# Performance work log

Measured on AMD Instinct MI355X. Metric: run time of the kernel, lower is better.

The kernel has to match this reference:

```python
import jax, jax.numpy as jnp
import numpy as np

N = 4096
C = 128
L = 4
E = 131072
HEADS = 4
BN_EPS = 1e-5


def setup_inputs() -> dict:
    key = jax.random.key(0)
    ks = jax.random.split(key, 16)
    s = jnp.float32(0.05)

    def rn(k, shape):
        return jax.random.normal(k, shape, dtype=jnp.float32) * s

    return {
        "x": jax.random.normal(ks[0], (N, C), dtype=jnp.float32),
        "edge_index": jax.random.randint(ks[1], (2, E), 0, N, dtype=jnp.int64) if jax.config.read("jax_enable_x64") else jax.random.randint(ks[1], (2, E), 0, N, dtype=jnp.int32),
        "gin_w1": rn(ks[2], (L, C, C)), "gin_b1": jnp.zeros((L, C), jnp.float32),
        "gin_w2": rn(ks[3], (L, C, C)), "gin_b2": jnp.zeros((L, C), jnp.float32),
        "attn_in_w": rn(ks[4], (L, 3 * C, C)), "attn_in_b": jnp.zeros((L, 3 * C), jnp.float32),
        "attn_out_w": rn(ks[5], (L, C, C)), "attn_out_b": jnp.zeros((L, C), jnp.float32),
        "n1_g": jnp.ones((L, C), jnp.float32), "n1_b": jnp.zeros((L, C), jnp.float32),
        "n2_g": jnp.ones((L, C), jnp.float32), "n2_b": jnp.zeros((L, C), jnp.float32),
        "n3_g": jnp.ones((L, C), jnp.float32), "n3_b": jnp.zeros((L, C), jnp.float32),
        "mlp_w1": rn(ks[6], (L, 2 * C, C)), "mlp_b1": jnp.zeros((L, 2 * C), jnp.float32),
        "mlp_w2": rn(ks[7], (L, C, 2 * C)), "mlp_b2": jnp.zeros((L, C), jnp.float32),
        "head_w1": rn(ks[8], (C // 2, C)), "head_b1": jnp.zeros((C // 2,), jnp.float32),
        "head_w2": rn(ks[9], (C // 4, C // 2)), "head_b2": jnp.zeros((C // 4,), jnp.float32),
        "head_w3": rn(ks[10], (1, C // 4)), "head_b3": jnp.zeros((1,), jnp.float32),
    }


def _bn(x, g, b):
    # BatchNorm1d over the node dim, training-mode (biased var), eps=1e-5
    mu = x.mean(axis=0)
    var = x.var(axis=0)
    return g * (x - mu) * jax.lax.rsqrt(var + BN_EPS) + b


def _gin(x, src, dst, w1, b1, w2, b2):
    # GINConv with eps=0: nn(x + sum_{j in N(i)} x_j)
    agg = jax.ops.segment_sum(x[src], dst, num_segments=x.shape[0])
    h = x + agg
    h = jnp.maximum(h @ w1.T + b1, 0.0)
    return h @ w2.T + b2


def _mha(x, wi, bi, wo, bo):
    # torch.nn.MultiheadAttention self-attention over a single dense batch of N nodes
    n, c = x.shape
    d = c // HEADS
    q, k, v = jnp.split(x @ wi.T + bi, 3, axis=-1)
    q = q.reshape(n, HEADS, d)
    k = k.reshape(n, HEADS, d)
    v = v.reshape(n, HEADS, d)
    scores = jnp.einsum('nhd,mhd->hnm', q, k) / jnp.sqrt(jnp.asarray(d, x.dtype))
    a = jax.nn.softmax(scores, axis=-1)
    o = jnp.einsum('hnm,mhd->nhd', a, v).reshape(n, c)
    return o @ wo.T + bo


def _forward(x, edge_index, gin_w1, gin_b1, gin_w2, gin_b2, attn_in_w, attn_in_b,
             attn_out_w, attn_out_b, n1_g, n1_b, n2_g, n2_b, n3_g, n3_b,
             mlp_w1, mlp_b1, mlp_w2, mlp_b2, head_w1, head_b1, head_w2, head_b2,
             head_w3, head_b3):
    src, dst = edge_index[0], edge_index[1]
    for i in range(L):
        # local GIN branch + residual + batch norm
        h1 = _bn(_gin(x, src, dst, gin_w1[i], gin_b1[i], gin_w2[i], gin_b2[i]) + x, n1_g[i], n1_b[i])
        # global attention branch + residual + batch norm
        h2 = _bn(_mha(x, attn_in_w[i], attn_in_b[i], attn_out_w[i], attn_out_b[i]) + x, n2_g[i], n2_b[i])
        h = h1 + h2
        # GPSConv MLP (C -> 2C -> C) with residual and final batch norm
        m = jnp.maximum(h @ mlp_w1[i].T + mlp_b1[i], 0.0) @ mlp_w2[i].T + mlp_b2[i]
        x = _bn(h + m, n3_g[i], n3_b[i])
    # head MLP: C -> C/2 -> C/4 -> 1
    h = jnp.maximum(x @ head_w1.T + head_b1, 0.0)
    h = jnp.maximum(h @ head_w2.T + head_b2, 0.0)
    return h @ head_w3.T + head_b3


def reference(x, edge_index, gin_w1, gin_b1, gin_w2, gin_b2, attn_in_w, attn_in_b,
              attn_out_w, attn_out_b, n1_g, n1_b, n2_g, n2_b, n3_g, n3_b,
              mlp_w1, mlp_b1, mlp_w2, mlp_b2, head_w1, head_b1, head_w2, head_b2,
              head_w3, head_b3):
    return _forward(x, edge_index, gin_w1, gin_b1, gin_w2, gin_b2, attn_in_w, attn_in_b,
                    attn_out_w, attn_out_b, n1_g, n1_b, n2_g, n2_b, n3_g, n3_b,
                    mlp_w1, mlp_b1, mlp_w2, mlp_b2, head_w1, head_b1, head_w2, head_b2,
                    head_w3, head_b3)
```

## Files before the change

kernel.cpp:

```cpp
#include <hip/hip_runtime.h>

#define N_NODES 4096
#define C_DIM   128
#define L_LAYERS 4
#define E_EDGES 131072
#define H_HEADS 4
#define D_HEAD  32
#define NC      (N_NODES * C_DIM)
#define NCu     (N_NODES * C_DIM)
#define P_STRIDE 136
#define HS_STRIDE 152
#define T2S       264

typedef short bf16x8 __attribute__((ext_vector_type(8)));
typedef float f32x4  __attribute__((ext_vector_type(4)));

__device__ __forceinline__ unsigned short f2bf(float f) {
    unsigned int u = __float_as_uint(f);
    u += 0x7fffu + ((u >> 16) & 1u);
    return (unsigned short)(u >> 16);
}

__device__ __forceinline__ float bf_lo(unsigned int u) { return __uint_as_float(u << 16); }
__device__ __forceinline__ float bf_hi(unsigned int u) { return __uint_as_float(u & 0xffff0000u); }

__device__ __forceinline__ bf16x8 pack8(const float* v) {
    bf16x8 o;
#pragma unroll
    for (int i = 0; i < 8; ++i) o[i] = (short)f2bf(v[i]);
    return o;
}

__global__ __launch_bounds__(256) void hist_kernel(const int* __restrict__ ei,
                                                   int* __restrict__ deg) {
    int e = blockIdx.x * 256 + threadIdx.x;
    atomicAdd(&deg[ei[E_EDGES + e]], 1);
}

__global__ __launch_bounds__(256) void scan_kernel(const int* __restrict__ deg,
                                                   int* __restrict__ rowstart,
                                                   int* __restrict__ cursor) {
    __shared__ int ts[256];
    const int tid = threadIdx.x;
    int loc[16];
    int s = 0;
#pragma unroll
    for (int i = 0; i < 16; ++i) { loc[i] = s; s += deg[tid * 16 + i]; }
    ts[tid] = s;
    __syncthreads();
    for (int off = 1; off < 256; off <<= 1) {
        int t = (tid >= off) ? ts[tid - off] : 0;
        __syncthreads();
        if (tid >= off) ts[tid] += t;
        __syncthreads();
    }
    int off0 = ts[tid] - s;
#pragma unroll
    for (int i = 0; i < 16; ++i) {
        int v = off0 + loc[i];
        rowstart[tid * 16 + i] = v;
        cursor[tid * 16 + i] = v;
    }
    if (tid == 255) rowstart[4096] = off0 + s;
}

__global__ __launch_bounds__(256) void fill_kernel(const int* __restrict__ ei,
                                                   int* __restrict__ cursor,
                                                   int* __restrict__ csr_src) {
    int e = blockIdx.x * 256 + threadIdx.x;
    int d = ei[E_EDGES + e];
    int s = ei[e];
    int p = atomicAdd(&cursor[d], 1);
    csr_src[p] = s;
}

__global__ __launch_bounds__(256) void wcvt(const float* __restrict__ s0, const float* __restrict__ s1,
                                            const float* __restrict__ s2, const float* __restrict__ s3,
                                            const float* __restrict__ s4, const float* __restrict__ s5,
                                            unsigned short* __restrict__ wbf) {
    int i0 = (blockIdx.x * 256 + threadIdx.x) * 8;
    const float* src; int base;
    if      (i0 < 65536)  { src = s0; base = 0; }
    else if (i0 < 131072) { src = s1; base = 65536; }
    else if (i0 < 327680) { src = s2; base = 131072; }
    else if (i0 < 393216) { src = s3; base = 327680; }
    else if (i0 < 524288) { src = s4; base = 393216; }
    else                  { src = s5; base = 524288; }
    const float* p = src + (i0 - base);
    float t[8];
#pragma unroll
    for (int i = 0; i < 8; ++i) t[i] = p[i];
    *(bf16x8*)(wbf + i0) = pack8(t);
}

__global__ __launch_bounds__(256) void x2bf(const float* __restrict__ x,
                                            unsigned short* __restrict__ xb) {
    int i0 = (blockIdx.x * 256 + threadIdx.x) * 8;
    float t[8];
#pragma unroll
    for (int i = 0; i < 8; ++i) t[i] = x[i0 + i];
    *(bf16x8*)(xb + i0) = pack8(t);
}

__global__ __launch_bounds__(256, 8) void qkv_gather(const unsigned short* __restrict__ xb,
                                                     const unsigned short* __restrict__ Wbf,
                                                     const float* __restrict__ bias,
                                                     unsigned short* __restrict__ Qb,
                                                     unsigned short* __restrict__ Kb,
                                                     unsigned short* __restrict__ VT,
                                                     const int* __restrict__ rowstart,
                                                     const int* __restrict__ csr_src,
                                                     unsigned int* __restrict__ hsum,
                                                     float* __restrict__ ssz) {
    const int b = blockIdx.x;
    const int tid = threadIdx.x;
    if (b < 1536) {
        const int ct = b % 6, rt = b / 6;
        const int wv = tid >> 6;
        const int lane = tid & 63, lg = lane >> 4, ll = lane & 15;
        const int rowbase = rt * 16;
        const int colbase = ct * 64 + wv * 16;

        const unsigned short* Ap = xb  + (size_t)(rowbase + ll) * 128 + lg * 8;
        const unsigned short* Wp = Wbf + (size_t)(colbase + ll) * 128 + lg * 8;

        f32x4 acc = {0.f, 0.f, 0.f, 0.f};
#pragma unroll
        for (int k = 0; k < 128; k += 32) {
            bf16x8 a = *(const bf16x8*)(Ap + k);
            bf16x8 w = *(const bf16x8*)(Wp + k);
            acc = __builtin_amdgcn_mfma_f32_16x16x32_bf16(a, w, acc, 0, 0, 0);
        }

        const float qsc = 0.25506973f;
        const int col = colbase + ll;
        const float bi = bias[col];
#pragma unroll
        for (int r = 0; r < 4; ++r) {
            const int row = rowbase + lg * 4 + r;
            float v = acc[r] + bi;
            if (col < 128) {
                int hh = col >> 5, d = col & 31;
                Qb[((size_t)hh * N_NODES + row) * D_HEAD + d] = f2bf(v * qsc);
            } else if (col < 256) {
                int c2 = col - 128, hh = c2 >> 5, d = c2 & 31;
                Kb[((size_t)hh * N_NODES + row) * D_HEAD + d] = f2bf(v);
            } else {
                int c2 = col - 256, hh = c2 >> 5, d = c2 & 31;
                VT[((size_t)hh * D_HEAD + d) * N_NODES + row] = f2bf(v);
            }
        }
    } else {
        if (b == 1536) {
            ssz[tid] = 0.f; ssz[256 + tid] = 0.f; ssz[512 + tid] = 0.f;
        }
        const int node = (b - 1536) * 4 + (tid >> 6);
        const int lane = tid & 63;
        const unsigned int* xu = (const unsigned int*)xb;
        const int beg = rowstart[node], end = rowstart[node + 1];
        unsigned int su = xu[(size_t)node * 64 + lane];
        float ax = bf_lo(su), ay = bf_hi(su);
        float bx = 0.f, by = 0.f;
        int e = beg;
        for (; e + 4 <= end; e += 4) {
            int s0 = csr_src[e], s1 = csr_src[e + 1], s2 = csr_src[e + 2], s3 = csr_src[e + 3];
            unsigned int u0 = xu[(size_t)s0 * 64 + lane];
            unsigned int u1 = xu[(size_t)s1 * 64 + lane];
            unsigned int u2 = xu[(size_t)s2 * 64 + lane];
            unsigned int u3 = xu[(size_t)s3 * 64 + lane];
            ax += bf_lo(u0) + bf_lo(u1); ay += bf_hi(u0) + bf_hi(u1);
            bx += bf_lo(u2) + bf_lo(u3); by += bf_hi(u2) + bf_hi(u3);
        }
        for (; e < end; ++e) {
            unsigned int u0 = xu[(size_t)csr_src[e] * 64 + lane];
            ax += bf_lo(u0); ay += bf_hi(u0);
        }
        float ox = ax + bx, oy = ay + by;
        hsum[(size_t)node * 64 + lane] = (unsigned int)f2bf(ox) | ((unsigned int)f2bf(oy) << 16);
    }
}

__global__ __launch_bounds__(512, 4) void attn_gin1(const unsigned short* __restrict__ Qb,
                                                    const unsigned short* __restrict__ Kb,
                                                    const unsigned short* __restrict__ VT,
                                                    unsigned short* __restrict__ ob,
                                                    const unsigned short* __restrict__ hsum,
                                                    const unsigned short* __restrict__ W1,
                                                    const float* __restrict__ bias1,
                                                    unsigned short* __restrict__ t1out) {
    __shared__ __align__(16) unsigned short Pl[8 * 32 * P_STRIDE];
    float (*Ouns)[32][33] = (float (*)[32][33])(void*)Pl;
    float (*Llp)[32] = (float (*)[32])(void*)(Pl + 8 * 32 * 33 * 2);

    const int b   = blockIdx.x;
    const int tid = threadIdx.x;
    const int wv  = tid >> 6;
    const int lane = tid & 63;
    const int lg  = lane >> 4;
    const int ll  = lane & 15;

    if (b >= 512) {
        const int rowbase = (b - 512) * 16;
        const int colbase = wv * 16;
        const unsigned short* Ap = hsum + (size_t)(rowbase + ll) * 128 + lg * 8;
        const unsigned short* Wp = W1 + (size_t)(colbase + ll) * 128 + lg * 8;
        f32x4 acc = {0.f, 0.f, 0.f, 0.f};
#pragma unroll
        for (int k = 0; k < 128; k += 32) {
            bf16x8 a = *(const bf16x8*)(Ap + k);
            bf16x8 w = *(const bf16x8*)(Wp + k);
            acc = __builtin_amdgcn_mfma_f32_16x16x32_bf16(a, w, acc, 0, 0, 0);
        }
        const int col = colbase + ll;
        const float bi = bias1[col];
#pragma unroll
        for (int r = 0; r < 4; ++r) {
            const int row = rowbase + lg * 4 + r;
            float v = fmaxf(acc[r] + bi, 0.f);
            t1out[(size_t)row * 128 + col] = f2bf(v);
        }
        return;
    }

    const int h   = b >> 7;
    const int q0  = (b & 127) * 32;

    const unsigned short* Qh = Qb + ((size_t)h * N_NODES + q0) * D_HEAD;
    const unsigned short* Kh = Kb + (size_t)h * N_NODES * D_HEAD;
    const unsigned short* Vh = VT + (size_t)h * D_HEAD * N_NODES;

    bf16x8 qf0 = *(const bf16x8*)(Qh + ll * D_HEAD + lg * 8);
    bf16x8 qf1 = *(const bf16x8*)(Qh + (16 + ll) * D_HEAD + lg * 8);

    f32x4 oacc00 = {0.f,0.f,0.f,0.f}, oacc01 = {0.f,0.f,0.f,0.f};
    f32x4 oacc10 = {0.f,0.f,0.f,0.f}, oacc11 = {0.f,0.f,0.f,0.f};
    float l0[4] = {0.f,0.f,0.f,0.f}, l1[4] = {0.f,0.f,0.f,0.f};

    unsigned short* Pw = Pl + wv * (32 * P_STRIDE);
    const int k0 = wv * (N_NODES / 8);

    for (int t = 0; t < (N_NODES / 8) / 128; ++t) {
        const int kt = k0 + t * 128;

        float s0[8][4], s1[8][4];
#pragma unroll
        for (int kc = 0; kc < 8; ++kc) {
            bf16x8 kf = *(const bf16x8*)(Kh + (size_t)(kt + kc * 16 + ll) * D_HEAD + lg * 8);
            f32x4 z = {0.f, 0.f, 0.f, 0.f};
            f32x4 d0 = __builtin_amdgcn_mfma_f32_16x16x32_bf16(qf0, kf, z, 0, 0, 0);
            f32x4 d1 = __builtin_amdgcn_mfma_f32_16x16x32_bf16(qf1, kf, z, 0, 0, 0);
#pragma unroll
            for (int r = 0; r < 4; ++r) { s0[kc][r] = d0[r]; s1[kc][r] = d1[r]; }
        }

#pragma unroll
        for (int r = 0; r < 4; ++r) {
            float a = 0.f, bb = 0.f;
#pragma unroll
            for (int kc = 0; kc < 8; ++kc) {
                float p0 = exp2f(s0[kc][r]); s0[kc][r] = p0; a += p0;
                float p1 = exp2f(s1[kc][r]); s1[kc][r] = p1; bb += p1;
            }
#pragma unroll
            for (int off = 1; off < 16; off <<= 1) {
                a += __shfl_xor(a, off, 64);
                bb += __shfl_xor(bb, off, 64);
            }
            l0[r] += a;
            l1[r] += bb;
        }

#pragma unroll
        for (int kc = 0; kc < 8; ++kc)
#pragma unroll
            for (int r = 0; r < 4; ++r) {
                Pw[(lg * 4 + r) * P_STRIDE + kc * 16 + ll]      = f2bf(s0[kc][r]);
                Pw[(16 + lg * 4 + r) * P_STRIDE + kc * 16 + ll] = f2bf(s1[kc][r]);
            }
        asm volatile("" ::: "memory");

#pragma unroll
        for (int kc2 = 0; kc2 < 4; ++kc2) {
            bf16x8 va = *(const bf16x8*)(Vh + (size_t)ll * N_NODES + kt + kc2 * 32 + lg * 8);
            bf16x8 vb = *(const bf16x8*)(Vh + (size_t)(16 + ll) * N_NODES + kt + kc2 * 32 + lg * 8);
            bf16x8 pf0 = *(const bf16x8*)(Pw + ll * P_STRIDE + kc2 * 32 + lg * 8);
            bf16x8 pf1 = *(const bf16x8*)(Pw + (16 + ll) * P_STRIDE + kc2 * 32 + lg * 8);
            oacc00 = __builtin_amdgcn_mfma_f32_16x16x32_bf16(pf0, va, oacc00, 0, 0, 0);
            oacc01 = __builtin_amdgcn_mfma_f32_16x16x32_bf16(pf0, vb, oacc01, 0, 0, 0);
            oacc10 = __builtin_amdgcn_mfma_f32_16x16x32_bf16(pf1, va, oacc10, 0, 0, 0);
            oacc11 = __builtin_amdgcn_mfma_f32_16x16x32_bf16(pf1, vb, oacc11, 0, 0, 0);
        }
    }

    __syncthreads();

#pragma unroll
    for (int r = 0; r < 4; ++r) {
        Ouns[wv][lg * 4 + r][ll]           = oacc00[r];
        Ouns[wv][lg * 4 + r][16 + ll]      = oacc01[r];
        Ouns[wv][16 + lg * 4 + r][ll]      = oacc10[r];
        Ouns[wv][16 + lg * 4 + r][16 + ll] = oacc11[r];
    }
    if (ll == 0) {
#pragma unroll
        for (int r = 0; r < 4; ++r) {
            Llp[wv][lg * 4 + r]      = l0[r];
            Llp[wv][16 + lg * 4 + r] = l1[r];
        }
    }
    __syncthreads();

    {
        const int row = tid >> 4, col = tid & 15;
        float L = 0.f, oa = 0.f, obv = 0.f;
#pragma unroll
        for (int w = 0; w < 8; ++w) {
            L   += Llp[w][row];
            oa  += Ouns[w][row][col];
            obv += Ouns[w][row][16 + col];
        }
        float inv = 1.f / L;
        ob[(size_t)(q0 + row) * C_DIM + h * D_HEAD + col]      = f2bf(oa * inv);
        ob[(size_t)(q0 + row) * C_DIM + h * D_HEAD + 16 + col] = f2bf(obv * inv);
    }
}

__global__ __launch_bounds__(256, 8) void gemm2x(const unsigned short* __restrict__ A0,
                                                 const unsigned short* __restrict__ W0,
                                                 const float* __restrict__ bias0,
                                                 float* __restrict__ out0,
                                                 float* __restrict__ stats0,
                                                 const unsigned short* __restrict__ A1,
                                                 const unsigned short* __restrict__ W1,
                                                 const float* __restrict__ bias1,
                                                 float* __restrict__ out1,
                                                 float* __restrict__ stats1,
                                                 const float* __restrict__ resid) {
    const int b = blockIdx.x;
    const int which = b >> 9;
    const int bl = b & 511;
    const unsigned short* Abf = which ? A1 : A0;
    const unsigned short* Wbf = which ? W1 : W0;
    const float* bias = which ? bias1 : bias0;
    float* outf  = which ? out1 : out0;
    float* stats = which ? stats1 : stats0;

    const int tid = threadIdx.x;
    const int wv = tid >> 6;
    const int lane = tid & 63, lg = lane >> 4, ll = lane & 15;
    const int rowbase = (bl >> 1) * 16;
    const int colbase = (bl & 1) * 64 + wv * 16;

    const unsigned short* Ap = Abf + (size_t)(rowbase + ll) * 128 + lg * 8;
    const unsigned short* Wp = Wbf + (size_t)(colbase + ll) * 128 + lg * 8;

    f32x4 acc = {0.f, 0.f, 0.f, 0.f};
#pragma unroll
    for (int k = 0; k < 128; k += 32) {
        bf16x8 a = *(const bf16x8*)(Ap + k);
        bf16x8 w = *(const bf16x8*)(Wp + k);
        acc = __builtin_amdgcn_mfma_f32_16x16x32_bf16(a, w, acc, 0, 0, 0);
    }

    const int col = colbase + ll;
    const float bi = bias[col];
    float sv = 0.f, sv2 = 0.f;
#pragma unroll
    for (int r = 0; r < 4; ++r) {
        const int row = rowbase + lg * 4 + r;
        float v = acc[r] + bi + resid[(size_t)row * 128 + col];
        outf[(size_t)row * 128 + col] = v;
        sv += v; sv2 += v * v;
    }
    sv  += __shfl_xor(sv, 16, 64);  sv  += __shfl_xor(sv, 32, 64);
    sv2 += __shfl_xor(sv2, 16, 64); sv2 += __shfl_xor(sv2, 32, 64);
    if (lg == 0) {
        atomicAdd(&stats[col], sv);
        atomicAdd(&stats[128 + col], sv2);
    }
}

__global__ __launch_bounds__(256) void mlp_fused(const float* __restrict__ g1p,
                                                 const float* __restrict__ a2p,
                                                 const float* __restrict__ st1,
                                                 const float* __restrict__ st2,
                                                 const float* __restrict__ g1v,
                                                 const float* __restrict__ b1v,
                                                 const float* __restrict__ g2v,
                                                 const float* __restrict__ b2v,
                                                 const unsigned short* __restrict__ W1bf,
                                                 const float* __restrict__ bias1,
                                                 const unsigned short* __restrict__ W2bf,
                                                 const float* __restrict__ bias2,
                                                 float* __restrict__ m3out,
                                                 float* __restrict__ stats3) {
    __shared__ float hf[16][132];
    __shared__ __align__(16) unsigned short hs[16 * HS_STRIDE];
    __shared__ __align__(16) unsigned short t2s[16 * T2S];
    __shared__ float scl[4][128];

    const int tid = threadIdx.x;
    const int rowbase = blockIdx.x * 16;
    const float inv_n = 1.f / N_NODES;

    if (tid < 128) {
        const int ch = tid;
        float m1 = st1[ch] * inv_n;
        float v1 = st1[128 + ch] * inv_n - m1 * m1;
        float r1 = rsqrtf(v1 + 1e-5f);
        float sc1 = g1v[ch] * r1;
        scl[0][ch] = sc1;
        scl[1][ch] = b1v[ch] - m1 * sc1;
        float m2 = st2[ch] * inv_n;
        float v2 = st2[128 + ch] * inv_n - m2 * m2;
        float r2 = rsqrtf(v2 + 1e-5f);
        float sc2 = g2v[ch] * r2;
        scl[2][ch] = sc2;
        scl[3][ch] = b2v[ch] - m2 * sc2;
    }
    __syncthreads();

#pragma unroll
    for (int j = tid; j < 512; j += 256) {
        const int r = j >> 5, cq = (j & 31) * 4;
        float4 v1 = *(const float4*)(g1p + (size_t)(rowbase + r) * 128 + cq);
        float4 v2 = *(const float4*)(a2p + (size_t)(rowbase + r) * 128 + cq);
        float h0 = v1.x * scl[0][cq]     + scl[1][cq]     + v2.x * scl[2][cq]     + scl[3][cq];
        float h1 = v1.y * scl[0][cq + 1] + scl[1][cq + 1] + v2.y * scl[2][cq + 1] + scl[3][cq + 1];
        float h2 = v1.z * scl[0][cq + 2] + scl[1][cq + 2] + v2.z * scl[2][cq + 2] + scl[3][cq + 2];
        float h3 = v1.w * scl[0][cq + 3] + scl[1][cq + 3] + v2.w * scl[2][cq + 3] + scl[3][cq + 3];
        hf[r][cq] = h0; hf[r][cq + 1] = h1; hf[r][cq + 2] = h2; hf[r][cq + 3] = h3;
        ushort4 u;
        u.x = f2bf(h0); u.y = f2bf(h1); u.z = f2bf(h2); u.w = f2bf(h3);
        *(ushort4*)(&hs[r * HS_STRIDE + cq]) = u;
    }
    __syncthreads();

    const int wv = tid >> 6;
    const int lane = tid & 63, lg = lane >> 4, ll = lane & 15;

#pragma unroll
    for (int ct = 0; ct < 4; ++ct) {
        const int colbase = wv * 16 + ct * 64;
        const unsigned short* Wp = W1bf + (size_t)(colbase + ll) * 128 + lg * 8;
        f32x4 acc = {0.f, 0.f, 0.f, 0.f};
#pragma unroll
        for (int k = 0; k < 128; k += 32) {
            bf16x8 a = *(const bf16x8*)(&hs[ll * HS_STRIDE + k + lg * 8]);
            bf16x8 w = *(const bf16x8*)(Wp + k);
            acc = __builtin_amdgcn_mfma_f32_16x16x32_bf16(a, w, acc, 0, 0, 0);
        }
        const int col = colbase + ll;
        const float bi = bias1[col];
#pragma unroll
        for (int r = 0; r < 4; ++r) {
            float v = fmaxf(acc[r] + bi, 0.f);
            t2s[(lg * 4 + r) * T2S + col] = f2bf(v);
        }
    }
    __syncthreads();

#pragma unroll
    for (int p = 0; p < 2; ++p) {
        const int colbase = p * 64 + wv * 16;
        const unsigned short* Wp = W2bf + (size_t)(colbase + ll) * 256 + lg * 8;
        f32x4 acc = {0.f, 0.f, 0.f, 0.f};
#pragma unroll
        for (int k = 0; k < 256; k += 32) {
            bf16x8 a = *(const bf16x8*)(&t2s[ll * T2S + k + lg * 8]);
            bf16x8 w = *(const bf16x8*)(Wp + k);
            acc = __builtin_amdgcn_mfma_f32_16x16x32_bf16(a, w, acc, 0, 0, 0);
        }
        const int col = colbase + ll;
        const float bi = bias2[col];
        float sv = 0.f, sv2 = 0.f;
#pragma unroll
        for (int r = 0; r < 4; ++r) {
            const int row = lg * 4 + r;
            float v = acc[r] + bi + hf[row][col];
            m3out[(size_t)(rowbase + row) * 128 + col] = v;
            sv += v; sv2 += v * v;
        }
        sv  += __shfl_xor(sv, 16, 64);  sv  += __shfl_xor(sv, 32, 64);
        sv2 += __shfl_xor(sv2, 16, 64); sv2 += __shfl_xor(sv2, 32, 64);
        if (lg == 0) {
            atomicAdd(&stats3[col], sv);
            atomicAdd(&stats3[128 + col], sv2);
        }
    }
}

__global__ __launch_bounds__(256) void bn_apply(const float* __restrict__ p,
                                                const float* __restrict__ st,
                                                const float* __restrict__ gv,
                                                const float* __restrict__ bv,
                                                float* __restrict__ out,
                                                unsigned short* __restrict__ outb) {
    int idx = blockIdx.x * 256 + threadIdx.x;
    int c4 = (idx & 31) * 4;
    const float inv_n = 1.f / N_NODES;
    float sc[4], sh[4];
#pragma unroll
    for (int c = 0; c < 4; ++c) {
        int ch = c4 + c;
        float m = st[ch] * inv_n;
        float vv = st[C_DIM + ch] * inv_n - m * m;
        float r = rsqrtf(vv + 1e-5f);
        sc[c] = gv[ch] * r; sh[c] = bv[ch] - m * sc[c];
    }
    float4 v = ((const float4*)p)[idx];
    float4 o;
    o.x = v.x * sc[0] + sh[0];
    o.y = v.y * sc[1] + sh[1];
    o.z = v.z * sc[2] + sh[2];
    o.w = v.w * sc[3] + sh[3];
    ((float4*)out)[idx] = o;
    ushort4 ub;
    ub.x = f2bf(o.x); ub.y = f2bf(o.y); ub.z = f2bf(o.z); ub.w = f2bf(o.w);
    *(ushort4*)(outb + (size_t)idx * 4) = ub;
}

__global__ __launch_bounds__(256) void head_fused(const float* __restrict__ x,
                                                  const float* __restrict__ w1,
                                                  const float* __restrict__ b1,
                                                  const float* __restrict__ w2,
                                                  const float* __restrict__ b2,
                                                  const float* __restrict__ w3,
                                                  const float* __restrict__ b3,
                                                  float* __restrict__ out) {
    __shared__ __align__(16) float xs[8][128];
    __shared__ __align__(16) float hs2[8][64];
    const int tid = threadIdx.x;
    const int n = tid >> 5;
    const int g = tid & 31;
    const int node0 = blockIdx.x * 8;

    {
        int r = tid >> 5, q = tid & 31;
        *(float4*)(&xs[r][q * 4]) = *(const float4*)(x + (size_t)(node0 + r) * 128 + q * 4);
    }
    __syncthreads();

    {
        float acc0 = b1[g], acc1 = b1[g + 32];
        const float* wa = w1 + (size_t)g * 128;
        const float* wb = w1 + (size_t)(g + 32) * 128;
#pragma unroll 8
        for (int k = 0; k < 128; k += 4) {
            float4 xv = *(const float4*)(&xs[n][k]);
            float4 va = *(const float4*)(wa + k);
            float4 vb = *(const float4*)(wb + k);
            acc0 += xv.x * va.x + xv.y * va.y + xv.z * va.z + xv.w * va.w;
            acc1 += xv.x * vb.x + xv.y * vb.y + xv.z * vb.z + xv.w * vb.w;
        }
        hs2[n][g]      = fmaxf(acc0, 0.f);
        hs2[n][g + 32] = fmaxf(acc1, 0.f);
    }
    __syncthreads();

    {
        float acc = b2[g];
        const float* wr = w2 + (size_t)g * 64;
#pragma unroll 8
        for (int k = 0; k < 64; k += 4) {
            float4 hv = *(const float4*)(&hs2[n][k]);
            float4 wv = *(const float4*)(wr + k);
            acc += hv.x * wv.x + hv.y * wv.y + hv.z * wv.z + hv.w * wv.w;
        }
        float t = fmaxf(acc, 0.f) * w3[g];
#pragma unroll
        for (int off = 1; off < 32; off <<= 1) t += __shfl_xor(t, off, 64);
        if (g == 0) out[node0 + n] = t + b3[0];
    }
}

extern "C" void kernel_launch(void* const* d_in, const int* in_sizes, int n_in,
                              void* d_out, int out_size, void* d_ws, size_t ws_size,
                              hipStream_t stream) {
    (void)in_sizes; (void)n_in; (void)out_size; (void)ws_size;
    const float* x_in   = (const float*)d_in[0];
    const int*   ei     = (const int*)d_in[1];
    const float* gin_w1 = (const float*)d_in[2];
    const float* gin_b1 = (const float*)d_in[3];
    const float* gin_w2 = (const float*)d_in[4];
    const float* gin_b2 = (const float*)d_in[5];
    const float* ain_w  = (const float*)d_in[6];
    const float* ain_b  = (const float*)d_in[7];
    const float* aout_w = (const float*)d_in[8];
    const float* aout_b = (const float*)d_in[9];
    const float* n1_g   = (const float*)d_in[10];
    const float* n1_b   = (const float*)d_in[11];
    const float* n2_g   = (const float*)d_in[12];
    const float* n2_b   = (const float*)d_in[13];
    const float* n3_g   = (const float*)d_in[14];
    const float* n3_b   = (const float*)d_in[15];
    const float* mlp_w1 = (const float*)d_in[16];
    const float* mlp_b1 = (const float*)d_in[17];
    const float* mlp_w2 = (const float*)d_in[18];
    const float* mlp_b2 = (const float*)d_in[19];
    const float* h_w1   = (const float*)d_in[20];
    const float* h_b1   = (const float*)d_in[21];
    const float* h_w2   = (const float*)d_in[22];
    const float* h_b2   = (const float*)d_in[23];
    const float* h_w3   = (const float*)d_in[24];
    const float* h_b3   = (const float*)d_in[25];

    float* f = (float*)d_ws;
    float* g1   = f;
    float* m3   = f;
    float* a2   = f + 1 * (size_t)NC;
    float* hbuf = f + 2 * (size_t)NC;
    float* xA   = f + 3 * (size_t)NC;
    float* xB   = f + 4 * (size_t)NC;
    unsigned short* R1  = (unsigned short*)(f + 5 * (size_t)NC);
    unsigned short* Qb      = R1;
    unsigned short* Kb      = R1 + (size_t)NCu;
    unsigned short* VT      = R1 + 2 * (size_t)NCu;
    unsigned short* R2      = R1 + 3 * (size_t)NCu;
    unsigned short* ao_bf   = R2;
    unsigned short* hsum_bf = (unsigned short*)a2;
    unsigned short* t1_bf   = (unsigned short*)hbuf;
    unsigned short* xbf     = R2 + (size_t)NCu;
    unsigned short* wbf     = xbf + (size_t)NCu;
    float* ss    = (float*)(wbf + 655360);
    int* ibase    = (int*)(ss + 768);
    int* deg      = ibase;
    int* rowstart = ibase + 4096;
    int* cursor   = ibase + 4096 + 4098;
    int* csr_src  = ibase + 4096 + 4098 + 4096;

    const int OG1 = 0, OG2 = 65536, OAI = 131072, OAO = 327680, OM1 = 393216, OM2 = 524288;

    hipMemsetAsync(deg, 0, 4096 * sizeof(int), stream);
    hist_kernel<<<E_EDGES / 256, 256, 0, stream>>>(ei, deg);
    scan_kernel<<<1, 256, 0, stream>>>(deg, rowstart, cursor);
    fill_kernel<<<E_EDGES / 256, 256, 0, stream>>>(ei, cursor, csr_src);
    wcvt<<<320, 256, 0, stream>>>(gin_w1, gin_w2, ain_w, aout_w, mlp_w1, mlp_w2, wbf);
    x2bf<<<NC / 2048, 256, 0, stream>>>(x_in, xbf);

    for (int i = 0; i < L_LAYERS; ++i) {
        const float* xin = (i == 0) ? x_in : ((i & 1) ? xA : xB);
        float* xout = (i & 1) ? xB : xA;
        const float* gb1 = gin_b1 + (size_t)i * C_DIM;
        const float* gb2 = gin_b2 + (size_t)i * C_DIM;
        const float* aib = ain_b + (size_t)i * 3 * C_DIM;
        const float* aob = aout_b + (size_t)i * C_DIM;
        const float* mb1 = mlp_b1 + (size_t)i * 2 * C_DIM;
        const float* mb2 = mlp_b2 + (size_t)i * C_DIM;

        qkv_gather<<<2560, 256, 0, stream>>>(xbf, wbf + OAI + (size_t)i * 49152, aib,
                                             Qb, Kb, VT, rowstart, csr_src,
                                             (unsigned int*)hsum_bf, ss);
        attn_gin1<<<768, 512, 0, stream>>>(Qb, Kb, VT, ao_bf,
                                           hsum_bf, wbf + OG1 + (size_t)i * 16384, gb1, t1_bf);
        gemm2x<<<1024, 256, 0, stream>>>(t1_bf, wbf + OG2 + (size_t)i * 16384, gb2, g1, ss,
                                         ao_bf, wbf + OAO + (size_t)i * 16384, aob, a2, ss + 256,
                                         xin);
        mlp_fused<<<256, 256, 0, stream>>>(g1, a2, ss, ss + 256,
                                           n1_g + (size_t)i * C_DIM, n1_b + (size_t)i * C_DIM,
                                           n2_g + (size_t)i * C_DIM, n2_b + (size_t)i * C_DIM,
                                           wbf + OM1 + (size_t)i * 32768, mb1,
                                           wbf + OM2 + (size_t)i * 32768, mb2,
                                           m3, ss + 512);
        bn_apply<<<512, 256, 0, stream>>>(m3, ss + 512,
                                          n3_g + (size_t)i * C_DIM, n3_b + (size_t)i * C_DIM,
                                          xout, xbf);
    }

    const float* xf = xB;
    head_fused<<<N_NODES / 8, 256, 0, stream>>>(xf, h_w1, h_b1, h_w2, h_b2, h_w3, h_b3,
                                                (float*)d_out);
}
```

Measured before the change: 383.5 us.

## Fold final batch-norm apply into next layer's consumers and drop bn_apply kernel

Removes the per-layer bn_apply kernel and the x2bf conversion. Consumers now read the raw pre-norm fp32 buffer m3 and apply the BN scale and shift on the fly: in the QKV GEMM (staged through LDS as bf16), in the GIN neighbor gather, in the residual of gemm2x, and in the head. Stats buffers are double-buffered so the previous layer's stats survive while the current layer accumulates its own. This saves one launch and a full read and write per layer, but the gather now reads fp32 rows (twice the bytes of bf16) and recomputes the scale and shift per block.

Measured after the change: 366.8 us. -4.4%, faster.

```diff
diff --git a/kernel.cpp b/kernel.cpp
--- a/kernel.cpp
+++ b/kernel.cpp
@@ -11,6 +11,7 @@
 #define P_STRIDE 136
 #define HS_STRIDE 152
 #define T2S       264
+#define AT_S      136
 
 typedef short bf16x8 __attribute__((ext_vector_type(8)));
 typedef float f32x4  __attribute__((ext_vector_type(4)));
@@ -93,16 +94,10 @@
     *(bf16x8*)(wbf + i0) = pack8(t);
 }
 
-__global__ __launch_bounds__(256) void x2bf(const float* __restrict__ x,
-                                            unsigned short* __restrict__ xb) {
-    int i0 = (blockIdx.x * 256 + threadIdx.x) * 8;
-    float t[8];
-#pragma unroll
-    for (int i = 0; i < 8; ++i) t[i] = x[i0 + i];
-    *(bf16x8*)(xb + i0) = pack8(t);
-}
-
-__global__ __launch_bounds__(256, 8) void qkv_gather(const unsigned short* __restrict__ xb,
+__global__ __launch_bounds__(256, 8) void qkv_gather(const float* __restrict__ xprev,
+                                                     const float* __restrict__ st3,
+                                                     const float* __restrict__ g3p,
+                                                     const float* __restrict__ b3p,
                                                      const unsigned short* __restrict__ Wbf,
                                                      const float* __restrict__ bias,
                                                      unsigned short* __restrict__ Qb,
@@ -110,24 +105,52 @@
                                                      unsigned short* __restrict__ VT,
                                                      const int* __restrict__ rowstart,
                                                      const int* __restrict__ csr_src,
-                                                     unsigned int* __restrict__ hsum,
-                                                     float* __restrict__ ssz) {
+                                                     float* __restrict__ ssz,
+                                                     unsigned int* __restrict__ hsum) {
+    __shared__ float scl2[2][128];
+    __shared__ __align__(16) unsigned short at[16 * AT_S];
+
     const int b = blockIdx.x;
     const int tid = threadIdx.x;
+    const float inv_n = 1.f / N_NODES;
+
     if (b < 1536) {
         const int ct = b % 6, rt = b / 6;
+        const int rowbase = rt * 16;
+
+        if (tid < 128) {
+            float sc = 1.f, sh = 0.f;
+            if (st3) {
+                float m = st3[tid] * inv_n;
+                float vv = st3[128 + tid] * inv_n - m * m;
+                float r = rsqrtf(vv + 1e-5f);
+                sc = g3p[tid] * r;
+                sh = b3p[tid] - m * sc;
+            }
+            scl2[0][tid] = sc; scl2[1][tid] = sh;
+        }
+        __syncthreads();
+
+        {
+            const int e0 = tid * 8;
+            const int r = e0 >> 7, c = e0 & 127;
+            const float* xp = xprev + (size_t)(rowbase + r) * 128 + c;
+            float t[8];
+#pragma unroll
+            for (int i = 0; i < 8; ++i) t[i] = xp[i] * scl2[0][c + i] + scl2[1][c + i];
+            *(bf16x8*)(&at[r * AT_S + c]) = pack8(t);
+        }
+        __syncthreads();
+
         const int wv = tid >> 6;
         const int lane = tid & 63, lg = lane >> 4, ll = lane & 15;
-        const int rowbase = rt * 16;
         const int colbase = ct * 64 + wv * 16;
-
-        const unsigned short* Ap = xb  + (size_t)(rowbase + ll) * 128 + lg * 8;
         const unsigned short* Wp = Wbf + (size_t)(colbase + ll) * 128 + lg * 8;
 
         f32x4 acc = {0.f, 0.f, 0.f, 0.f};
 #pragma unroll
         for (int k = 0; k < 128; k += 32) {
-            bf16x8 a = *(const bf16x8*)(Ap + k);
+            bf16x8 a = *(const bf16x8*)(&at[ll * AT_S + k + lg * 8]);
             bf16x8 w = *(const bf16x8*)(Wp + k);
             acc = __builtin_amdgcn_mfma_f32_16x16x32_bf16(a, w, acc, 0, 0, 0);
         }
@@ -156,24 +179,37 @@
         }
         const int node = (b - 1536) * 4 + (tid >> 6);
         const int lane = tid & 63;
-        const unsigned int* xu = (const unsigned int*)xb;
+        const int ch0 = lane * 2, ch1 = ch0 + 1;
+        float sc0 = 1.f, sh0 = 0.f, sc1 = 1.f, sh1 = 0.f;
+        if (st3) {
+            float m0 = st3[ch0] * inv_n;
+            float v0 = st3[128 + ch0] * inv_n - m0 * m0;
+            float r0 = rsqrtf(v0 + 1e-5f);
+            sc0 = g3p[ch0] * r0; sh0 = b3p[ch0] - m0 * sc0;
+            float m1 = st3[ch1] * inv_n;
+            float v1 = st3[128 + ch1] * inv_n - m1 * m1;
+            float r1 = rsqrtf(v1 + 1e-5f);
+            sc1 = g3p[ch1] * r1; sh1 = b3p[ch1] - m1 * sc1;
+        }
         const int beg = rowstart[node], end = rowstart[node + 1];
-        unsigned int su = xu[(size_t)node * 64 + lane];
-        float ax = bf_lo(su), ay = bf_hi(su);
+        float2 sv = *(const float2*)(xprev + (size_t)node * 128 + ch0);
+        float ax = sv.x * sc0 + sh0, ay = sv.y * sc1 + sh1;
         float bx = 0.f, by = 0.f;
         int e = beg;
         for (; e + 4 <= end; e += 4) {
             int s0 = csr_src[e], s1 = csr_src[e + 1], s2 = csr_src[e + 2], s3 = csr_src[e + 3];
-            unsigned int u0 = xu[(size_t)s0 * 64 + lane];
-            unsigned int u1 = xu[(size_t)s1 * 64 + lane];
-            unsigned int u2 = xu[(size_t)s2 * 64 + lane];
-            unsigned int u3 = xu[(size_t)s3 * 64 + lane];
-            ax += bf_lo(u0) + bf_lo(u1); ay += bf_hi(u0) + bf_hi(u1);
-            bx += bf_lo(u2) + bf_lo(u3); by += bf_hi(u2) + bf_hi(u3);
+            float2 v0 = *(const float2*)(xprev + (size_t)s0 * 128 + ch0);
+            float2 v1 = *(const float2*)(xprev + (size_t)s1 * 128 + ch0);
+            float2 v2 = *(const float2*)(xprev + (size_t)s2 * 128 + ch0);
+            float2 v3 = *(const float2*)(xprev + (size_t)s3 * 128 + ch0);
+            ax += (v0.x * sc0 + sh0) + (v1.x * sc0 + sh0);
+            ay += (v0.y * sc1 + sh1) + (v1.y * sc1 + sh1);
+            bx += (v2.x * sc0 + sh0) + (v3.x * sc0 + sh0);
+            by += (v2.y * sc1 + sh1) + (v3.y * sc1 + sh1);
         }
         for (; e < end; ++e) {
-            unsigned int u0 = xu[(size_t)csr_src[e] * 64 + lane];
-            ax += bf_lo(u0); ay += bf_hi(u0);
+            float2 v0 = *(const float2*)(xprev + (size_t)csr_src[e] * 128 + ch0);
+            ax += v0.x * sc0 + sh0; ay += v0.y * sc1 + sh1;
         }
         float ox = ax + bx, oy = ay + by;
         hsum[(size_t)node * 64 + lane] = (unsigned int)f2bf(ox) | ((unsigned int)f2bf(oy) << 16);
@@ -335,7 +371,10 @@
                                                  const float* __restrict__ bias1,
                                                  float* __restrict__ out1,
                                                  float* __restrict__ stats1,
-                                                 const float* __restrict__ resid) {
+                                                 const float* __restrict__ xprev,
+                                                 const float* __restrict__ st3,
+                                                 const float* __restrict__ g3p,
+                                                 const float* __restrict__ b3p) {
     const int b = blockIdx.x;
     const int which = b >> 9;
     const int bl = b & 511;
@@ -364,11 +403,19 @@
 
     const int col = colbase + ll;
     const float bi = bias[col];
+    float sc = 1.f, sh = 0.f;
+    if (st3) {
+        const float inv_n = 1.f / N_NODES;
+        float m = st3[col] * inv_n;
+        float vv = st3[128 + col] * inv_n - m * m;
+        float r = rsqrtf(vv + 1e-5f);
+        sc = g3p[col] * r; sh = b3p[col] - m * sc;
+    }
     float sv = 0.f, sv2 = 0.f;
 #pragma unroll
     for (int r = 0; r < 4; ++r) {
         const int row = rowbase + lg * 4 + r;
-        float v = acc[r] + bi + resid[(size_t)row * 128 + col];
+        float v = acc[r] + bi + (xprev[(size_t)row * 128 + col] * sc + sh);
         outf[(size_t)row * 128 + col] = v;
         sv += v; sv2 += v * v;
     }
@@ -490,37 +537,10 @@
     }
 }
 
-__global__ __launch_bounds__(256) void bn_apply(const float* __restrict__ p,
-                                                const float* __restrict__ st,
-                                                const float* __restrict__ gv,
-                                                const float* __restrict__ bv,
-                                                float* __restrict__ out,
-                                                unsigned short* __restrict__ outb) {
-    int idx = blockIdx.x * 256 + threadIdx.x;
-    int c4 = (idx & 31) * 4;
-    const float inv_n = 1.f / N_NODES;
-    float sc[4], sh[4];
-#pragma unroll
-    for (int c = 0; c < 4; ++c) {
-        int ch = c4 + c;
-        float m = st[ch] * inv_n;
-        float vv = st[C_DIM + ch] * inv_n - m * m;
-        float r = rsqrtf(vv + 1e-5f);
-        sc[c] = gv[ch] * r; sh[c] = bv[ch] - m * sc[c];
-    }
-    float4 v = ((const float4*)p)[idx];
-    float4 o;
-    o.x = v.x * sc[0] + sh[0];
-    o.y = v.y * sc[1] + sh[1];
-    o.z = v.z * sc[2] + sh[2];
-    o.w = v.w * sc[3] + sh[3];
-    ((float4*)out)[idx] = o;
-    ushort4 ub;
-    ub.x = f2bf(o.x); ub.y = f2bf(o.y); ub.z = f2bf(o.z); ub.w = f2bf(o.w);
-    *(ushort4*)(outb + (size_t)idx * 4) = ub;
-}
-
-__global__ __launch_bounds__(256) void head_fused(const float* __restrict__ x,
+__global__ __launch_bounds__(256) void head_fused(const float* __restrict__ m3p,
+                                                  const float* __restrict__ st3,
+                                                  const float* __restrict__ g3p,
+                                                  const float* __restrict__ b3p,
                                                   const float* __restrict__ w1,
                                                   const float* __restrict__ b1,
                                                   const float* __restrict__ w2,
@@ -530,14 +550,31 @@
                                                   float* __restrict__ out) {
     __shared__ __align__(16) float xs[8][128];
     __shared__ __align__(16) float hs2[8][64];
+    __shared__ float scl2[2][128];
     const int tid = threadIdx.x;
     const int n = tid >> 5;
     const int g = tid & 31;
     const int node0 = blockIdx.x * 8;
+    const float inv_n = 1.f / N_NODES;
+
+    if (tid < 128) {
+        float m = st3[tid] * inv_n;
+        float vv = st3[128 + tid] * inv_n - m * m;
+        float r = rsqrtf(vv + 1e-5f);
+        float sc = g3p[tid] * r;
+        scl2[0][tid] = sc;
+        scl2[1][tid] = b3p[tid] - m * sc;
+    }
+    __syncthreads();
 
     {
-        int r = tid >> 5, q = tid & 31;
-        *(float4*)(&xs[r][q * 4]) = *(const float4*)(x + (size_t)(node0 + r) * 128 + q * 4);
+        const int e0 = tid * 4;
+        const int r = e0 >> 7, c = e0 & 127;
+        float4 v = *(const float4*)(m3p + (size_t)(node0 + r) * 128 + c);
+        xs[r][c]     = v.x * scl2[0][c]     + scl2[1][c];
+        xs[r][c + 1] = v.y * scl2[0][c + 1] + scl2[1][c + 1];
+        xs[r][c + 2] = v.z * scl2[0][c + 2] + scl2[1][c + 2];
+        xs[r][c + 3] = v.w * scl2[0][c + 3] + scl2[1][c + 3];
     }
     __syncthreads();
 
@@ -607,23 +644,21 @@
 
     float* f = (float*)d_ws;
     float* g1   = f;
-    float* m3   = f;
     float* a2   = f + 1 * (size_t)NC;
-    float* hbuf = f + 2 * (size_t)NC;
-    float* xA   = f + 3 * (size_t)NC;
-    float* xB   = f + 4 * (size_t)NC;
-    unsigned short* R1  = (unsigned short*)(f + 5 * (size_t)NC);
+    float* t1ch = f + 2 * (size_t)NC;
+    float* m3   = f + 3 * (size_t)NC;
+    unsigned short* R1  = (unsigned short*)(f + 4 * (size_t)NC);
     unsigned short* Qb      = R1;
     unsigned short* Kb      = R1 + (size_t)NCu;
     unsigned short* VT      = R1 + 2 * (size_t)NCu;
     unsigned short* R2      = R1 + 3 * (size_t)NCu;
     unsigned short* ao_bf   = R2;
     unsigned short* hsum_bf = (unsigned short*)a2;
-    unsigned short* t1_bf   = (unsigned short*)hbuf;
-    unsigned short* xbf     = R2 + (size_t)NCu;
-    unsigned short* wbf     = xbf + (size_t)NCu;
-    float* ss    = (float*)(wbf + 655360);
-    int* ibase    = (int*)(ss + 768);
+    unsigned short* t1_bf   = (unsigned short*)t1ch;
+    unsigned short* wbf     = R2 + (size_t)NCu;
+    float* ssA    = (float*)(wbf + 655360);
+    float* ssB    = ssA + 768;
+    int* ibase    = (int*)(ssB + 768);
     int* deg      = ibase;
     int* rowstart = ibase + 4096;
     int* cursor   = ibase + 4096 + 4098;
@@ -636,11 +671,13 @@
     scan_kernel<<<1, 256, 0, stream>>>(deg, rowstart, cursor);
     fill_kernel<<<E_EDGES / 256, 256, 0, stream>>>(ei, cursor, csr_src);
     wcvt<<<320, 256, 0, stream>>>(gin_w1, gin_w2, ain_w, aout_w, mlp_w1, mlp_w2, wbf);
-    x2bf<<<NC / 2048, 256, 0, stream>>>(x_in, xbf);
 
     for (int i = 0; i < L_LAYERS; ++i) {
-        const float* xin = (i == 0) ? x_in : ((i & 1) ? xA : xB);
-        float* xout = (i & 1) ? xB : xA;
+        const float* xprev = (i == 0) ? x_in : m3;
+        const float* st3p  = (i == 0) ? nullptr : ((i & 1) ? ssA : ssB) + 512;
+        const float* g3p   = (i == 0) ? nullptr : n3_g + (size_t)(i - 1) * C_DIM;
+        const float* b3p   = (i == 0) ? nullptr : n3_b + (size_t)(i - 1) * C_DIM;
+        float* ss_cur = (i & 1) ? ssB : ssA;
         const float* gb1 = gin_b1 + (size_t)i * C_DIM;
         const float* gb2 = gin_b2 + (size_t)i * C_DIM;
         const float* aib = ain_b + (size_t)i * 3 * C_DIM;
@@ -648,26 +685,25 @@
         const float* mb1 = mlp_b1 + (size_t)i * 2 * C_DIM;
         const float* mb2 = mlp_b2 + (size_t)i * C_DIM;
 
-        qkv_gather<<<2560, 256, 0, stream>>>(xbf, wbf + OAI + (size_t)i * 49152, aib,
+        qkv_gather<<<2560, 256, 0, stream>>>(xprev, st3p, g3p, b3p,
+                                             wbf + OAI + (size_t)i * 49152, aib,
                                              Qb, Kb, VT, rowstart, csr_src,
-                                             (unsigned int*)hsum_bf, ss);
+                                             ss_cur, (unsigned int*)hsum_bf);
         attn_gin1<<<768, 512, 0, stream>>>(Qb, Kb, VT, ao_bf,
                                            hsum_bf, wbf + OG1 + (size_t)i * 16384, gb1, t1_bf);
-        gemm2x<<<1024, 256, 0, stream>>>(t1_bf, wbf + OG2 + (size_t)i * 16384, gb2, g1, ss,
-                                         ao_bf, wbf + OAO + (size_t)i * 16384, aob, a2, ss + 256,
-                                         xin);
-        mlp_fused<<<256, 256, 0, stream>>>(g1, a2, ss, ss + 256,
+        gemm2x<<<1024, 256, 0, stream>>>(t1_bf, wbf + OG2 + (size_t)i * 16384, gb2, g1, ss_cur,
+                                         ao_bf, wbf + OAO + (size_t)i * 16384, aob, a2, ss_cur + 256,
+                                         xprev, st3p, g3p, b3p);
+        mlp_fused<<<256, 256, 0, stream>>>(g1, a2, ss_cur, ss_cur + 256,
                                            n1_g + (size_t)i * C_DIM, n1_b + (size_t)i * C_DIM,
                                            n2_g + (size_t)i * C_DIM, n2_b + (size_t)i * C_DIM,
                                            wbf + OM1 + (size_t)i * 32768, mb1,
                                            wbf + OM2 + (size_t)i * 32768, mb2,
-                                           m3, ss + 512);
-        bn_apply<<<512, 256, 0, stream>>>(m3, ss + 512,
-                                          n3_g + (size_t)i * C_DIM, n3_b + (size_t)i * C_DIM,
-                                          xout, xbf);
-    }
-
-    const float* xf = xB;
-    head_fused<<<N_NODES / 8, 256, 0, stream>>>(xf, h_w1, h_b1, h_w2, h_b2, h_w3, h_b3,
+                                           m3, ss_cur + 512);
+    }
+
+    head_fused<<<N_NODES / 8, 256, 0, stream>>>(m3, ssB + 512,
+                                                n3_g + 3 * (size_t)C_DIM, n3_b + 3 * (size_t)C_DIM,
+                                                h_w1, h_b1, h_w2, h_b2, h_w3, h_b3,
                                                 (float*)d_out);
 }
```
